# Performance work log

Measured on AMD Instinct MI355X. Metric: run time of the kernel, lower is better.

The kernel has to match this reference:

```python
import jax, jax.numpy as jnp
import numpy as np

N, E, F_IN = 12288, 196608, 1433


def setup_inputs() -> dict:
    key = jax.random.key(0)
    ks = jax.random.split(key, 11)
    inp = {
        "x": jax.random.normal(ks[0], (N, F_IN), dtype=jnp.float32),
        "edge_index": jax.random.randint(ks[1], (2, E), 0, N, dtype=jnp.int64),
        "W1": jax.random.normal(ks[2], (F_IN, 32), dtype=jnp.float32) * 0.02,
        "b1": jnp.zeros((32,), dtype=jnp.float32),
        "Wl": jax.random.normal(ks[3], (32, 16), dtype=jnp.float32) * 0.1,
        "bl": jnp.zeros((16,), dtype=jnp.float32),
        "Wr": jax.random.normal(ks[4], (32, 16), dtype=jnp.float32) * 0.1,
        "br": jnp.zeros((16,), dtype=jnp.float32),
        "W3": jax.random.normal(ks[5], (16, 7), dtype=jnp.float32) * 0.1,
        "b3": jnp.zeros((7,), dtype=jnp.float32),
    }
    return inp


def reference(x, edge_index, W1, b1, Wl, bl, Wr, br, W3, b3):
    n = x.shape[0]
    loops = jnp.arange(n, dtype=edge_index.dtype)
    row = jnp.concatenate([edge_index[0], loops])  # [E+N]
    col = jnp.concatenate([edge_index[1], loops])

    # ---- GCN layer: dense symmetric-normalized adjacency (faithful to original) ----
    # degree computed over the col index of self-looped edges
    deg = jnp.zeros((n,), dtype=x.dtype).at[col].add(1.0)
    dis = jnp.where(deg > 0, deg ** -0.5, 0.0)  # inf -> 0 guard
    A = jnp.zeros((n, n), dtype=x.dtype).at[row, col].add(1.0)  # dense A-hat
    A_norm = dis[:, None] * A * dis[None, :]  # D^-1/2 A D^-1/2
    h = (A_norm @ x) @ W1 + b1
    h = jax.nn.relu(h)  # [N, 32]

    # ---- GraphSAGE layer: mean over neighbors j with edge (i -> j) ----
    src, dst = edge_index[0], edge_index[1]
    agg_sum = jax.ops.segment_sum(h[dst], src, num_segments=n)  # [N, 32]
    cnt = jax.ops.segment_sum(jnp.ones((src.shape[0],), dtype=h.dtype), src, num_segments=n)
    agg = jnp.where(cnt[:, None] > 0, agg_sum / jnp.maximum(cnt, 1.0)[:, None], 0.0)
    out = jax.nn.relu(h @ Wl + bl + agg @ Wr + br)  # [N, 16]
    out = out / (jnp.linalg.norm(out, axis=1, keepdims=True) + 1e-6)

    # ---- head: linear + dropout(eval: identity) + softmax ----
    logits = out @ W3 + b3  # [N, 7]
    return jax.nn.softmax(logits, axis=1)
```

## Files before the change

### kernel.cpp

```cpp
#include <hip/hip_runtime.h>
#include <math.h>

#define GN 12288
#define GE 196608
#define GK 1433
#define GC 32
#define CAP 64
#define NCHUNK 45
#define NGRP 180
#define GEMMB 768
#define EDGEB 768
#define PACKB 23
#define ZEROB 96

typedef __attribute__((ext_vector_type(8))) short bf16x8;
typedef __attribute__((ext_vector_type(4))) float f32x4;

static __device__ inline unsigned short f2bf(float f) {
    unsigned u = __float_as_uint(f);
    return (unsigned short)((u + 0x7fffu + ((u >> 16) & 1u)) >> 16);
}
static __device__ inline float bf2f(unsigned short h) {
    return __uint_as_float(((unsigned)h) << 16);
}

__global__ __launch_bounds__(256) void prep_kernel(const float* __restrict__ W1,
                                                   unsigned* __restrict__ zbuf,
                                                   unsigned short* __restrict__ Whb,
                                                   unsigned short* __restrict__ Wlb) {
    int t = threadIdx.x, b = blockIdx.x;
    if (b < PACKB) {
        int idx = b * 256 + t;
        if (idx < NGRP * GC) {
            int g = idx >> 5, c = idx & 31;
            bf16x8 vh, vl;
            #pragma unroll
            for (int j = 0; j < 8; ++j) {
                int k = g * 8 + j;
                float f = (k < GK) ? W1[(size_t)k * GC + c] : 0.f;
                unsigned short hh = f2bf(f);
                vh[j] = (short)hh;
                vl[j] = (short)f2bf(f - bf2f(hh));
            }
            *(bf16x8*)(Whb + (size_t)idx * 8) = vh;
            *(bf16x8*)(Wlb + (size_t)idx * 8) = vl;
        }
    } else {
        int idx = (b - PACKB) * 256 + t;
        zbuf[idx] = 0u;
    }
}

__global__ __launch_bounds__(256) void fused_kernel(const float* __restrict__ x,
                                                    const int* __restrict__ ei,
                                                    const unsigned short* __restrict__ Whb,
                                                    const unsigned short* __restrict__ Wlb,
                                                    float* __restrict__ xw,
                                                    unsigned* __restrict__ cnt,
                                                    unsigned* __restrict__ deg,
                                                    unsigned* __restrict__ adjF) {
    int t = threadIdx.x, bid = blockIdx.x;

    if (bid >= GEMMB) {
        int e = (bid - GEMMB) * 256 + t;
        int src = ei[e];
        int dst = ei[GE + e];
        unsigned pos = atomicAdd(&cnt[src], 1u);
        if (pos < CAP) adjF[(unsigned)src * CAP + pos] = (unsigned)dst;
        atomicAdd(&deg[dst], 1u);
        return;
    }

    __shared__ float red[4][16][32];
    int lane = t & 63, w = t >> 6;
    int quad = lane >> 4, l15 = lane & 15;
    int row = bid * 16 + l15;
    const float* xr = x + (size_t)row * GK;
    f32x4 acc0 = {}, acc1 = {};
    int qs = w * 12;
    int qe = min(NCHUNK, qs + 12);

    float aA[8], aB[8];
    bf16x8 hA0, hA1, lA0, lA1, hB0, hB1, lB0, lB1;

#define LOADX(A8, q) { \
    int kq = (q) * 32 + quad * 8; \
    const float* p = xr + kq; \
    if (kq + 8 <= GK) { \
        _Pragma("unroll") for (int j = 0; j < 8; ++j) A8[j] = p[j]; \
    } else { \
        _Pragma("unroll") for (int j = 0; j < 8; ++j) A8[j] = (kq + j < GK) ? p[j] : 0.f; \
    } }

#define LOADW(H0, H1, L0, L1, q) { \
    int g = (q) * 4 + quad; \
    H0 = *(const bf16x8*)(Whb + (size_t)g * 256 + l15 * 8); \
    H1 = *(const bf16x8*)(Whb + (size_t)g * 256 + 128 + l15 * 8); \
    L0 = *(const bf16x8*)(Wlb + (size_t)g * 256 + l15 * 8); \
    L1 = *(const bf16x8*)(Wlb + (size_t)g * 256 + 128 + l15 * 8); \
    }

#define COMP(A8, H0, H1, L0, L1) { \
    bf16x8 ah, al; \
    _Pragma("unroll") for (int j = 0; j < 8; ++j) { \
        unsigned short hh = f2bf(A8[j]); \
        ah[j] = (short)hh; \
        al[j] = (short)f2bf(A8[j] - bf2f(hh)); \
    } \
    acc0 = __builtin_amdgcn_mfma_f32_16x16x32_bf16(ah, H0, acc0, 0, 0, 0); \
    acc1 = __builtin_amdgcn_mfma_f32_16x16x32_bf16(ah, H1, acc1, 0, 0, 0); \
    acc0 = __builtin_amdgcn_mfma_f32_16x16x32_bf16(ah, L0, acc0, 0, 0, 0); \
    acc1 = __builtin_amdgcn_mfma_f32_16x16x32_bf16(ah, L1, acc1, 0, 0, 0); \
    acc0 = __builtin_amdgcn_mfma_f32_16x16x32_bf16(al, H0, acc0, 0, 0, 0); \
    acc1 = __builtin_amdgcn_mfma_f32_16x16x32_bf16(al, H1, acc1, 0, 0, 0); \
    }

    int q = qs;
    LOADX(aA, q); LOADW(hA0, hA1, lA0, lA1, q);
    while (true) {
        if (q + 1 < qe) { LOADX(aB, q + 1); LOADW(hB0, hB1, lB0, lB1, q + 1); }
        COMP(aA, hA0, hA1, lA0, lA1);
        ++q; if (q >= qe) break;
        if (q + 1 < qe) { LOADX(aA, q + 1); LOADW(hA0, hA1, lA0, lA1, q + 1); }
        COMP(aB, hB0, hB1, lB0, lB1);
        ++q; if (q >= qe) break;
    }

    #pragma unroll
    for (int i = 0; i < 4; ++i) {
        red[w][quad * 4 + i][l15] = acc0[i];
        red[w][quad * 4 + i][16 + l15] = acc1[i];
    }
    __syncthreads();
    int r0 = t >> 5, c0 = t & 31;
    float s0 = red[0][r0][c0] + red[1][r0][c0] + red[2][r0][c0] + red[3][r0][c0];
    int r1 = r0 + 8;
    float s1 = red[0][r1][c0] + red[1][r1][c0] + red[2][r1][c0] + red[3][r1][c0];
    xw[(size_t)bid * 512 + t] = s0;
    xw[(size_t)bid * 512 + 256 + t] = s1;
}

__global__ __launch_bounds__(256) void gcn_kernel(const float* __restrict__ xw,
                                                  const unsigned* __restrict__ deg,
                                                  const unsigned* __restrict__ cnt,
                                                  const unsigned* __restrict__ adjF,
                                                  const float* __restrict__ b1,
                                                  float* __restrict__ h) {
    int w = threadIdx.x >> 6;
    int lane = threadIdx.x & 63;
    int i = blockIdx.x * 4 + w;
    int f = lane & 31, half = lane >> 5;
    unsigned cl = min(cnt[i], (unsigned)CAP);
    const unsigned* ai = adjF + (unsigned)i * CAP;
    float acc = 0.f;
    for (unsigned j = half; j < cl; j += 8) {
        unsigned lim = cl - 1;
        unsigned j1 = j + 2, j2 = j + 4, j3 = j + 6;
        unsigned d0 = ai[j];
        unsigned d1 = ai[min(j1, lim)];
        unsigned d2 = ai[min(j2, lim)];
        unsigned d3 = ai[min(j3, lim)];
        float m1 = j1 < cl ? 1.f : 0.f;
        float m2 = j2 < cl ? 1.f : 0.f;
        float m3 = j3 < cl ? 1.f : 0.f;
        acc += xw[(size_t)d0 * GC + f] * rsqrtf((float)(deg[d0] + 1u));
        acc += m1 * xw[(size_t)d1 * GC + f] * rsqrtf((float)(deg[d1] + 1u));
        acc += m2 * xw[(size_t)d2 * GC + f] * rsqrtf((float)(deg[d2] + 1u));
        acc += m3 * xw[(size_t)d3 * GC + f] * rsqrtf((float)(deg[d3] + 1u));
    }
    acc += __shfl_xor(acc, 32, 64);
    float disi = rsqrtf((float)(deg[i] + 1u));
    float v = b1[f] + disi * (disi * xw[(size_t)i * GC + f] + acc);
    if (half == 0) h[(size_t)i * GC + f] = fmaxf(v, 0.f);
}

__global__ __launch_bounds__(256) void sage_kernel(const float* __restrict__ h,
                                                   const unsigned* __restrict__ cnt,
                                                   const unsigned* __restrict__ adjF,
                                                   const float* __restrict__ Wl,
                                                   const float* __restrict__ bl,
                                                   const float* __restrict__ Wr,
                                                   const float* __restrict__ br,
                                                   const float* __restrict__ W3,
                                                   const float* __restrict__ b3,
                                                   float* __restrict__ out) {
    __shared__ float sh[4][64];
    __shared__ float so[4][16];
    int w = threadIdx.x >> 6, lane = threadIdx.x & 63;
    int i = blockIdx.x * 4 + w;
    int f = lane & 31, half = lane >> 5;
    unsigned ci = cnt[i];
    unsigned cl = min(ci, (unsigned)CAP);
    const unsigned* ai = adjF + (unsigned)i * CAP;
    float acc = 0.f;
    for (unsigned j = half; j < cl; j += 8) {
        unsigned lim = cl - 1;
        unsigned j1 = j + 2, j2 = j + 4, j3 = j + 6;
        unsigned d0 = ai[j];
        unsigned d1 = ai[min(j1, lim)];
        unsigned d2 = ai[min(j2, lim)];
        unsigned d3 = ai[min(j3, lim)];
        float m1 = j1 < cl ? 1.f : 0.f;
        float m2 = j2 < cl ? 1.f : 0.f;
        float m3 = j3 < cl ? 1.f : 0.f;
        acc += h[(size_t)d0 * GC + f];
        acc += m1 * h[(size_t)d1 * GC + f];
        acc += m2 * h[(size_t)d2 * GC + f];
        acc += m3 * h[(size_t)d3 * GC + f];
    }
    acc += __shfl_xor(acc, 32, 64);
    float agg = ci ? acc / (float)ci : 0.f;
    float hv = h[(size_t)i * GC + f];
    if (half == 0) { sh[w][f] = hv; sh[w][32 + f] = agg; }
    __syncthreads();
    int c = lane;
    float hid = 0.f;
    if (c < 16) {
        hid = bl[c] + br[c];
        #pragma unroll
        for (int ff = 0; ff < 32; ++ff)
            hid += sh[w][ff] * Wl[ff * 16 + c] + sh[w][32 + ff] * Wr[ff * 16 + c];
        hid = fmaxf(hid, 0.f);
    }
    float n2 = hid * hid;
    n2 += __shfl_xor(n2, 1, 64);
    n2 += __shfl_xor(n2, 2, 64);
    n2 += __shfl_xor(n2, 4, 64);
    n2 += __shfl_xor(n2, 8, 64);
    float o = hid / (sqrtf(n2) + 1e-6f);
    if (c < 16) so[w][c] = o;
    __syncthreads();
    float logit = -INFINITY;
    if (lane < 7) {
        logit = b3[lane];
        #pragma unroll
        for (int cc = 0; cc < 16; ++cc) logit += so[w][cc] * W3[cc * 7 + lane];
    }
    float m = logit;
    m = fmaxf(m, __shfl_xor(m, 1, 64));
    m = fmaxf(m, __shfl_xor(m, 2, 64));
    m = fmaxf(m, __shfl_xor(m, 4, 64));
    float e = expf(logit - m);
    float s = e;
    s += __shfl_xor(s, 1, 64);
    s += __shfl_xor(s, 2, 64);
    s += __shfl_xor(s, 4, 64);
    if (lane < 7) out[(size_t)i * 7 + lane] = e / s;
}

extern "C" void kernel_launch(void* const* d_in, const int* in_sizes, int n_in,
                              void* d_out, int out_size, void* d_ws, size_t ws_size,
                              hipStream_t stream) {
    const float* x  = (const float*)d_in[0];
    const int*   ei = (const int*)d_in[1];
    const float* W1 = (const float*)d_in[2];
    const float* b1 = (const float*)d_in[3];
    const float* Wl = (const float*)d_in[4];
    const float* bl = (const float*)d_in[5];
    const float* Wr = (const float*)d_in[6];
    const float* br = (const float*)d_in[7];
    const float* W3 = (const float*)d_in[8];
    const float* b3 = (const float*)d_in[9];
    float* out = (float*)d_out;

    char* ws = (char*)d_ws;
    const size_t S = (size_t)GN * GC * 4;
    float*    xw   = (float*)(ws);
    unsigned* cnt  = (unsigned*)(ws + S);
    unsigned* deg  = cnt + GN;
    float*    h    = (float*)(deg + GN);
    unsigned* adjF = (unsigned*)((char*)h + S);
    unsigned short* Whb = (unsigned short*)((char*)adjF + (size_t)GN * CAP * 4);
    unsigned short* Wlb = Whb + (size_t)NGRP * GC * 8;

    prep_kernel<<<PACKB + ZEROB, 256, 0, stream>>>(W1, cnt, Whb, Wlb);
    fused_kernel<<<GEMMB + EDGEB, 256, 0, stream>>>(x, ei, Whb, Wlb, xw, cnt, deg, adjF);
    gcn_kernel<<<GN / 4, 256, 0, stream>>>(xw, deg, cnt, adjF, b1, h);
    sage_kernel<<<GN / 4, 256, 0, stream>>>(h, cnt, adjF, Wl, bl, Wr, br, W3, b3, out);
}
```

Baseline: 164.7 us.

## Split edge and GEMM kernels, deepen GEMM prefetch pipeline to four stages

Splits the fused GEMM-plus-edge kernel into two kernels: an edge-scatter kernel and a dedicated GEMM kernel. The GEMM now balances the 45 K-chunks across its four waves instead of giving 12/12/12/9, and it prefetches three chunks ahead with four register buffers instead of double buffering. The deeper pipeline puts more global loads in flight to hide the latency of streaming x. In exchange it uses more registers, which may lower occupancy, and adds one more kernel launch.

```diff
diff --git a/kernel.cpp b/kernel.cpp
--- a/kernel.cpp
+++ b/kernel.cpp
@@ -51,37 +51,37 @@
     }
 }
 
-__global__ __launch_bounds__(256) void fused_kernel(const float* __restrict__ x,
-                                                    const int* __restrict__ ei,
-                                                    const unsigned short* __restrict__ Whb,
-                                                    const unsigned short* __restrict__ Wlb,
-                                                    float* __restrict__ xw,
-                                                    unsigned* __restrict__ cnt,
-                                                    unsigned* __restrict__ deg,
-                                                    unsigned* __restrict__ adjF) {
+__global__ __launch_bounds__(256) void edge_kernel(const int* __restrict__ ei,
+                                                   unsigned* __restrict__ cnt,
+                                                   unsigned* __restrict__ deg,
+                                                   unsigned* __restrict__ adjF) {
+    int e = blockIdx.x * 256 + threadIdx.x;
+    int src = ei[e];
+    int dst = ei[GE + e];
+    unsigned pos = atomicAdd(&cnt[src], 1u);
+    if (pos < CAP) adjF[(unsigned)src * CAP + pos] = (unsigned)dst;
+    atomicAdd(&deg[dst], 1u);
+}
+
+__global__ __launch_bounds__(256) void gemm_kernel(const float* __restrict__ x,
+                                                   const unsigned short* __restrict__ Whb,
+                                                   const unsigned short* __restrict__ Wlb,
+                                                   float* __restrict__ xw) {
+    __shared__ float red[4][16][32];
     int t = threadIdx.x, bid = blockIdx.x;
-
-    if (bid >= GEMMB) {
-        int e = (bid - GEMMB) * 256 + t;
-        int src = ei[e];
-        int dst = ei[GE + e];
-        unsigned pos = atomicAdd(&cnt[src], 1u);
-        if (pos < CAP) adjF[(unsigned)src * CAP + pos] = (unsigned)dst;
-        atomicAdd(&deg[dst], 1u);
-        return;
-    }
-
-    __shared__ float red[4][16][32];
     int lane = t & 63, w = t >> 6;
     int quad = lane >> 4, l15 = lane & 15;
     int row = bid * 16 + l15;
     const float* xr = x + (size_t)row * GK;
     f32x4 acc0 = {}, acc1 = {};
-    int qs = w * 12;
-    int qe = min(NCHUNK, qs + 12);
-
-    float aA[8], aB[8];
-    bf16x8 hA0, hA1, lA0, lA1, hB0, hB1, lB0, lB1;
+    int qs = (w * NCHUNK) >> 2;
+    int qe = ((w + 1) * NCHUNK) >> 2;
+
+    float aA[8], aB[8], aC[8], aD[8];
+    bf16x8 hA0, hA1, lA0, lA1;
+    bf16x8 hB0, hB1, lB0, lB1;
+    bf16x8 hC0, hC1, lC0, lC1;
+    bf16x8 hD0, hD1, lD0, lD1;
 
 #define LOADX(A8, q) { \
     int kq = (q) * 32 + quad * 8; \
@@ -116,13 +116,21 @@
     }
 
     int q = qs;
-    LOADX(aA, q); LOADW(hA0, hA1, lA0, lA1, q);
+    LOADX(aA, q);     LOADW(hA0, hA1, lA0, lA1, q);
+    LOADX(aB, q + 1); LOADW(hB0, hB1, lB0, lB1, q + 1);
+    LOADX(aC, q + 2); LOADW(hC0, hC1, lC0, lC1, q + 2);
     while (true) {
-        if (q + 1 < qe) { LOADX(aB, q + 1); LOADW(hB0, hB1, lB0, lB1, q + 1); }
+        if (q + 3 < qe) { LOADX(aD, q + 3); LOADW(hD0, hD1, lD0, lD1, q + 3); }
         COMP(aA, hA0, hA1, lA0, lA1);
         ++q; if (q >= qe) break;
-        if (q + 1 < qe) { LOADX(aA, q + 1); LOADW(hA0, hA1, lA0, lA1, q + 1); }
+        if (q + 3 < qe) { LOADX(aA, q + 3); LOADW(hA0, hA1, lA0, lA1, q + 3); }
         COMP(aB, hB0, hB1, lB0, lB1);
+        ++q; if (q >= qe) break;
+        if (q + 3 < qe) { LOADX(aB, q + 3); LOADW(hB0, hB1, lB0, lB1, q + 3); }
+        COMP(aC, hC0, hC1, lC0, lC1);
+        ++q; if (q >= qe) break;
+        if (q + 3 < qe) { LOADX(aC, q + 3); LOADW(hC0, hC1, lC0, lC1, q + 3); }
+        COMP(aD, hD0, hD1, lD0, lD1);
         ++q; if (q >= qe) break;
     }
 
@@ -274,7 +282,8 @@
     unsigned short* Wlb = Whb + (size_t)NGRP * GC * 8;
 
     prep_kernel<<<PACKB + ZEROB, 256, 0, stream>>>(W1, cnt, Whb, Wlb);
-    fused_kernel<<<GEMMB + EDGEB, 256, 0, stream>>>(x, ei, Whb, Wlb, xw, cnt, deg, adjF);
+    edge_kernel<<<EDGEB, 256, 0, stream>>>(ei, cnt, deg, adjF);
+    gemm_kernel<<<GEMMB, 256, 0, stream>>>(x, Whb, Wlb, xw);
     gcn_kernel<<<GN / 4, 256, 0, stream>>>(xw, deg, cnt, adjF, b1, h);
     sage_kernel<<<GN / 4, 256, 0, stream>>>(h, cnt, adjF, Wl, bl, Wr, br, W3, b3, out);
 }
```

Result: slower. 173.4 us (+5.3%).

## Stage x tiles through LDS with coalesced float4 loads in GEMM

Applied to the files above, without the earlier changes.

The dense x@W1 GEMM no longer has each lane read 8 strided floats directly from its own row. The block now loads 16-row by 512-column slabs of x with coalesced 16-byte loads into a padded LDS tile, prefetching the next slab while computing the current one. Each wave then reads its K-slice from LDS. Bf16 conversion switches to the hardware intrinsic, and the packed-weight padding grows to 192 groups. This aims to improve global memory coalescing for the bandwidth-bound x read, at the cost of extra LDS traffic and barriers.

```diff
diff --git a/kernel.cpp b/kernel.cpp
--- a/kernel.cpp
+++ b/kernel.cpp
@@ -1,4 +1,5 @@
 #include <hip/hip_runtime.h>
+#include <hip/hip_bf16.h>
 #include <math.h>
 
 #define GN 12288
@@ -6,15 +7,16 @@
 #define GK 1433
 #define GC 32
 #define CAP 64
-#define NCHUNK 45
-#define NGRP 180
+#define NGRP 192
 #define GEMMB 768
 #define EDGEB 768
-#define PACKB 23
+#define PACKB 24
 #define ZEROB 96
+#define XSTR 516
 
 typedef __attribute__((ext_vector_type(8))) short bf16x8;
 typedef __attribute__((ext_vector_type(4))) float f32x4;
+typedef float f32x4a __attribute__((ext_vector_type(4), aligned(4)));
 
 static __device__ inline unsigned short f2bf(float f) {
     unsigned u = __float_as_uint(f);
@@ -22,6 +24,9 @@
 }
 static __device__ inline float bf2f(unsigned short h) {
     return __uint_as_float(((unsigned)h) << 16);
+}
+static __device__ inline unsigned short f2bf_hw(float f) {
+    return __builtin_bit_cast(unsigned short, __float2bfloat16(f));
 }
 
 __global__ __launch_bounds__(256) void prep_kernel(const float* __restrict__ W1,
@@ -31,20 +36,18 @@
     int t = threadIdx.x, b = blockIdx.x;
     if (b < PACKB) {
         int idx = b * 256 + t;
-        if (idx < NGRP * GC) {
-            int g = idx >> 5, c = idx & 31;
-            bf16x8 vh, vl;
-            #pragma unroll
-            for (int j = 0; j < 8; ++j) {
-                int k = g * 8 + j;
-                float f = (k < GK) ? W1[(size_t)k * GC + c] : 0.f;
-                unsigned short hh = f2bf(f);
-                vh[j] = (short)hh;
-                vl[j] = (short)f2bf(f - bf2f(hh));
-            }
-            *(bf16x8*)(Whb + (size_t)idx * 8) = vh;
-            *(bf16x8*)(Wlb + (size_t)idx * 8) = vl;
+        int g = idx >> 5, c = idx & 31;
+        bf16x8 vh, vl;
+        #pragma unroll
+        for (int j = 0; j < 8; ++j) {
+            int k = g * 8 + j;
+            float f = (k < GK) ? W1[(size_t)k * GC + c] : 0.f;
+            unsigned short hh = f2bf(f);
+            vh[j] = (short)hh;
+            vl[j] = (short)f2bf(f - bf2f(hh));
         }
+        *(bf16x8*)(Whb + (size_t)idx * 8) = vh;
+        *(bf16x8*)(Wlb + (size_t)idx * 8) = vl;
     } else {
         int idx = (b - PACKB) * 256 + t;
         zbuf[idx] = 0u;
@@ -71,71 +74,107 @@
         return;
     }
 
-    __shared__ float red[4][16][32];
+    __shared__ __align__(16) float xs[16][XSTR];
     int lane = t & 63, w = t >> 6;
     int quad = lane >> 4, l15 = lane & 15;
-    int row = bid * 16 + l15;
-    const float* xr = x + (size_t)row * GK;
+    const float* xb = x + (size_t)bid * 16 * GK;
     f32x4 acc0 = {}, acc1 = {};
-    int qs = w * 12;
-    int qe = min(NCHUNK, qs + 12);
-
-    float aA[8], aB[8];
-    bf16x8 hA0, hA1, lA0, lA1, hB0, hB1, lB0, lB1;
-
-#define LOADX(A8, q) { \
-    int kq = (q) * 32 + quad * 8; \
-    const float* p = xr + kq; \
-    if (kq + 8 <= GK) { \
-        _Pragma("unroll") for (int j = 0; j < 8; ++j) A8[j] = p[j]; \
-    } else { \
-        _Pragma("unroll") for (int j = 0; j < 8; ++j) A8[j] = (kq + j < GK) ? p[j] : 0.f; \
+
+    int r0 = t >> 7;
+    int pos = t & 127;
+    f32x4 g0, g1, g2, g3, g4, g5, g6, g7;
+
+#define LOADG(K0) { \
+    const float* pp = xb + (size_t)r0 * GK + (K0) + pos * 4; \
+    g0 = *(const f32x4a*)(pp); \
+    g1 = *(const f32x4a*)(pp + 2 * GK); \
+    g2 = *(const f32x4a*)(pp + 4 * GK); \
+    g3 = *(const f32x4a*)(pp + 6 * GK); \
+    g4 = *(const f32x4a*)(pp + 8 * GK); \
+    g5 = *(const f32x4a*)(pp + 10 * GK); \
+    g6 = *(const f32x4a*)(pp + 12 * GK); \
+    g7 = *(const f32x4a*)(pp + 14 * GK); }
+
+#define LG1(DST, ROFF, PP, KB) { \
+    const float* q_ = (PP) + (size_t)(ROFF) * GK; \
+    if ((KB) + 4 <= GK) DST = *(const f32x4a*)q_; \
+    else { \
+        DST[0] = ((KB) + 0 < GK) ? q_[0] : 0.f; \
+        DST[1] = ((KB) + 1 < GK) ? q_[1] : 0.f; \
+        DST[2] = ((KB) + 2 < GK) ? q_[2] : 0.f; \
+        DST[3] = ((KB) + 3 < GK) ? q_[3] : 0.f; } }
+
+#define LOADG_TAIL(K0) { \
+    const float* pp = xb + (size_t)r0 * GK + (K0) + pos * 4; \
+    int kb = (K0) + pos * 4; \
+    LG1(g0, 0, pp, kb)  LG1(g1, 2, pp, kb)  LG1(g2, 4, pp, kb)  LG1(g3, 6, pp, kb) \
+    LG1(g4, 8, pp, kb)  LG1(g5, 10, pp, kb) LG1(g6, 12, pp, kb) LG1(g7, 14, pp, kb) }
+
+#define STOREL() { \
+    float* lp = &xs[r0][pos * 4]; \
+    *(f32x4*)(lp)              = g0; \
+    *(f32x4*)(lp + 2 * XSTR)   = g1; \
+    *(f32x4*)(lp + 4 * XSTR)   = g2; \
+    *(f32x4*)(lp + 6 * XSTR)   = g3; \
+    *(f32x4*)(lp + 8 * XSTR)   = g4; \
+    *(f32x4*)(lp + 10 * XSTR)  = g5; \
+    *(f32x4*)(lp + 12 * XSTR)  = g6; \
+    *(f32x4*)(lp + 14 * XSTR)  = g7; }
+
+#define COMPUTE(S) { \
+    _Pragma("unroll") \
+    for (int c = 0; c < 4; ++c) { \
+        int kl = w * 128 + c * 32 + quad * 8; \
+        const float* ap = &xs[l15][kl]; \
+        f32x4 x0 = *(const f32x4*)ap; \
+        f32x4 x1 = *(const f32x4*)(ap + 4); \
+        bf16x8 ah, al; \
+        _Pragma("unroll") for (int j = 0; j < 4; ++j) { \
+            unsigned short hh = f2bf_hw(x0[j]); \
+            ah[j] = (short)hh; al[j] = (short)f2bf_hw(x0[j] - bf2f(hh)); } \
+        _Pragma("unroll") for (int j = 0; j < 4; ++j) { \
+            unsigned short hh = f2bf_hw(x1[j]); \
+            ah[4 + j] = (short)hh; al[4 + j] = (short)f2bf_hw(x1[j] - bf2f(hh)); } \
+        int gg = (S) * 64 + w * 16 + c * 4 + quad; \
+        bf16x8 H0 = *(const bf16x8*)(Whb + (size_t)gg * 256 + l15 * 8); \
+        bf16x8 H1 = *(const bf16x8*)(Whb + (size_t)gg * 256 + 128 + l15 * 8); \
+        bf16x8 L0 = *(const bf16x8*)(Wlb + (size_t)gg * 256 + l15 * 8); \
+        bf16x8 L1 = *(const bf16x8*)(Wlb + (size_t)gg * 256 + 128 + l15 * 8); \
+        acc0 = __builtin_amdgcn_mfma_f32_16x16x32_bf16(ah, H0, acc0, 0, 0, 0); \
+        acc1 = __builtin_amdgcn_mfma_f32_16x16x32_bf16(ah, H1, acc1, 0, 0, 0); \
+        acc0 = __builtin_amdgcn_mfma_f32_16x16x32_bf16(ah, L0, acc0, 0, 0, 0); \
+        acc1 = __builtin_amdgcn_mfma_f32_16x16x32_bf16(ah, L1, acc1, 0, 0, 0); \
+        acc0 = __builtin_amdgcn_mfma_f32_16x16x32_bf16(al, H0, acc0, 0, 0, 0); \
+        acc1 = __builtin_amdgcn_mfma_f32_16x16x32_bf16(al, H1, acc1, 0, 0, 0); \
     } }
 
-#define LOADW(H0, H1, L0, L1, q) { \
-    int g = (q) * 4 + quad; \
-    H0 = *(const bf16x8*)(Whb + (size_t)g * 256 + l15 * 8); \
-    H1 = *(const bf16x8*)(Whb + (size_t)g * 256 + 128 + l15 * 8); \
-    L0 = *(const bf16x8*)(Wlb + (size_t)g * 256 + l15 * 8); \
-    L1 = *(const bf16x8*)(Wlb + (size_t)g * 256 + 128 + l15 * 8); \
-    }
-
-#define COMP(A8, H0, H1, L0, L1) { \
-    bf16x8 ah, al; \
-    _Pragma("unroll") for (int j = 0; j < 8; ++j) { \
-        unsigned short hh = f2bf(A8[j]); \
-        ah[j] = (short)hh; \
-        al[j] = (short)f2bf(A8[j] - bf2f(hh)); \
-    } \
-    acc0 = __builtin_amdgcn_mfma_f32_16x16x32_bf16(ah, H0, acc0, 0, 0, 0); \
-    acc1 = __builtin_amdgcn_mfma_f32_16x16x32_bf16(ah, H1, acc1, 0, 0, 0); \
-    acc0 = __builtin_amdgcn_mfma_f32_16x16x32_bf16(ah, L0, acc0, 0, 0, 0); \
-    acc1 = __builtin_amdgcn_mfma_f32_16x16x32_bf16(ah, L1, acc1, 0, 0, 0); \
-    acc0 = __builtin_amdgcn_mfma_f32_16x16x32_bf16(al, H0, acc0, 0, 0, 0); \
-    acc1 = __builtin_amdgcn_mfma_f32_16x16x32_bf16(al, H1, acc1, 0, 0, 0); \
-    }
-
-    int q = qs;
-    LOADX(aA, q); LOADW(hA0, hA1, lA0, lA1, q);
-    while (true) {
-        if (q + 1 < qe) { LOADX(aB, q + 1); LOADW(hB0, hB1, lB0, lB1, q + 1); }
-        COMP(aA, hA0, hA1, lA0, lA1);
-        ++q; if (q >= qe) break;
-        if (q + 1 < qe) { LOADX(aA, q + 1); LOADW(hA0, hA1, lA0, lA1, q + 1); }
-        COMP(aB, hB0, hB1, lB0, lB1);
-        ++q; if (q >= qe) break;
-    }
-
+    LOADG(0);
+    STOREL();
+    __syncthreads();
+    LOADG(512);
+    COMPUTE(0);
+    __syncthreads();
+    STOREL();
+    __syncthreads();
+    LOADG_TAIL(1024);
+    COMPUTE(1);
+    __syncthreads();
+    STOREL();
+    __syncthreads();
+    COMPUTE(2);
+    __syncthreads();
+
+    float (*red)[16][32] = (float (*)[16][32])(&xs[0][0]);
     #pragma unroll
     for (int i = 0; i < 4; ++i) {
         red[w][quad * 4 + i][l15] = acc0[i];
         red[w][quad * 4 + i][16 + l15] = acc1[i];
     }
     __syncthreads();
-    int r0 = t >> 5, c0 = t & 31;
-    float s0 = red[0][r0][c0] + red[1][r0][c0] + red[2][r0][c0] + red[3][r0][c0];
-    int r1 = r0 + 8;
-    float s1 = red[0][r1][c0] + red[1][r1][c0] + red[2][r1][c0] + red[3][r1][c0];
+    int rr0 = t >> 5, cc0 = t & 31;
+    float s0 = red[0][rr0][cc0] + red[1][rr0][cc0] + red[2][rr0][cc0] + red[3][rr0][cc0];
+    int rr1 = rr0 + 8;
+    float s1 = red[0][rr1][cc0] + red[1][rr1][cc0] + red[2][rr1][cc0] + red[3][rr1][cc0];
     xw[(size_t)bid * 512 + t] = s0;
     xw[(size_t)bid * 512 + 256 + t] = s1;
 }
```

Result: faster. 154.1 us (-6.4%).
